# Kernel tuning notes

Hardware: AMD Instinct MI355X
Metric: run time of the kernel (lower is better)

## Reference

```python
import jax, jax.numpy as jnp
import numpy as np

D_MODEL = 512
NHEAD = 8
HEAD_DIM = D_MODEL // NHEAD


def setup_inputs() -> dict:
    key = jax.random.key(0)
    k1, k2, k3, k4, k5 = jax.random.split(key, 5)
    x = jax.random.normal(k1, (4, 2048, D_MODEL), dtype=jnp.float32)
    s = 1.0 / np.sqrt(D_MODEL)
    W_qkv = jax.random.normal(k2, (D_MODEL, 3 * D_MODEL), dtype=jnp.float32) * s
    b_qkv = jax.random.normal(k3, (3 * D_MODEL,), dtype=jnp.float32) * 0.01
    W_fc = jax.random.normal(k4, (D_MODEL, D_MODEL), dtype=jnp.float32) * s
    b_fc = jax.random.normal(k5, (D_MODEL,), dtype=jnp.float32) * 0.01
    return {"x": x, "W_qkv": W_qkv, "b_qkv": b_qkv, "W_fc": W_fc, "b_fc": b_fc}


def reference(x, W_qkv, b_qkv, W_fc, b_fc):
    b, t, _ = x.shape
    qkv = x @ W_qkv + b_qkv                      # [b, t, 3*d]
    q, k, v = jnp.split(qkv, 3, axis=-1)
    def heads(a):
        return a.reshape(b, t, NHEAD, HEAD_DIM).transpose(0, 2, 1, 3)  # b h t d
    q, k, v = heads(q), heads(k), heads(v)
    scale = HEAD_DIM ** -0.5
    dots = jnp.einsum('bhid,bhjd->bhij', q, k) * scale
    attn = jax.nn.softmax(dots, axis=-1)         # dropout = identity (eval)
    out = jnp.einsum('bhij,bhjd->bhid', attn, v)
    out = out.transpose(0, 2, 1, 3).reshape(b, t, D_MODEL)
    return out @ W_fc + b_fc
```

## Files before the change

### kernel.cpp

```cpp
#include <hip/hip_runtime.h>
#include <hip/hip_bf16.h>
#include <cstddef>
#include <cstdint>

typedef __bf16 bf16_t;
typedef __attribute__((ext_vector_type(8))) __bf16 bf16x8;
typedef __attribute__((ext_vector_type(4))) float f32x4;
typedef __attribute__((ext_vector_type(16))) float f32x16;
typedef __attribute__((ext_vector_type(2))) unsigned uint2v;

#define B_   4
#define T_   2048
#define D_   512
#define H_   8
#define HD_  64
#define BT_  8192
#define N3_  1536

__device__ inline f32x4 mfma16(bf16x8 a, bf16x8 b, f32x4 c) {
  return __builtin_amdgcn_mfma_f32_16x16x32_bf16(a, b, c, 0, 0, 0);
}
__device__ inline f32x16 mfma32(bf16x8 a, bf16x8 b, f32x16 c) {
  return __builtin_amdgcn_mfma_f32_32x32x16_bf16(a, b, c, 0, 0, 0);
}


__global__ __launch_bounds__(256) void k_tcast(const float* __restrict__ in,
                                               bf16_t* __restrict__ out,
                                               int R, int C) {
  __shared__ bf16_t tile[64][72];
  const int c0 = blockIdx.x * 64, r0 = blockIdx.y * 64;
  const int t = threadIdx.x;
  const int rr = t >> 4;
  const int cc = (t & 15) * 4;
#pragma unroll
  for (int p = 0; p < 4; ++p) {
    int r = p * 16 + rr;
    f32x4 v = *reinterpret_cast<const f32x4*>(&in[(size_t)(r0 + r) * C + c0 + cc]);
#pragma unroll
    for (int i = 0; i < 4; ++i) tile[cc + i][r] = (bf16_t)v[i];
  }
  __syncthreads();
#pragma unroll
  for (int p = 0; p < 4; ++p) {
    int c = p * 16 + rr;
    union { uint2 u; bf16_t e[4]; } pk;
#pragma unroll
    for (int i = 0; i < 4; ++i) pk.e[i] = tile[c][cc + i];
    *reinterpret_cast<uint2*>(&out[(size_t)(c0 + c) * R + r0 + cc]) = pk.u;
  }
}

__global__ __launch_bounds__(256) void k_gemm_qkv(
    const float* __restrict__ X, const bf16_t* __restrict__ Wt,
    const float* __restrict__ bias, bf16_t* __restrict__ Qp,
    bf16_t* __restrict__ Kp, bf16_t* __restrict__ Vp) {
  __shared__ bf16_t As[128][40];
  __shared__ bf16_t Bs[128][40];
  const int bm0 = blockIdx.x * 128, bn0 = blockIdx.y * 128;
  const int tid = threadIdx.x, lane = tid & 63, wid = tid >> 6;
  const int wm = wid >> 1, wn = wid & 1;
  const int srow = tid >> 1, sh = (tid & 1) * 16;
  f32x4 acc[4][4] = {};
  for (int kt = 0; kt < D_; kt += 32) {
    {
      const float* s = &X[(size_t)(bm0 + srow) * D_ + kt + sh];
      f32x4 v0 = *reinterpret_cast<const f32x4*>(s);
      f32x4 v1 = *reinterpret_cast<const f32x4*>(s + 4);
      f32x4 v2 = *reinterpret_cast<const f32x4*>(s + 8);
      f32x4 v3 = *reinterpret_cast<const f32x4*>(s + 12);
      bf16x8 lo, hi;
#pragma unroll
      for (int i = 0; i < 4; ++i) {
        lo[i] = (bf16_t)v0[i]; lo[4 + i] = (bf16_t)v1[i];
        hi[i] = (bf16_t)v2[i]; hi[4 + i] = (bf16_t)v3[i];
      }
      *reinterpret_cast<bf16x8*>(&As[srow][sh]) = lo;
      *reinterpret_cast<bf16x8*>(&As[srow][sh + 8]) = hi;
    }
    {
      const bf16_t* s = &Wt[(size_t)(bn0 + srow) * D_ + kt + sh];
      *reinterpret_cast<bf16x8*>(&Bs[srow][sh]) =
          *reinterpret_cast<const bf16x8*>(s);
      *reinterpret_cast<bf16x8*>(&Bs[srow][sh + 8]) =
          *reinterpret_cast<const bf16x8*>(s + 8);
    }
    __syncthreads();
    const int fr = lane & 15, kq = (lane >> 4) * 8;
    bf16x8 af[4], bfr[4];
#pragma unroll
    for (int m = 0; m < 4; ++m)
      af[m] = *reinterpret_cast<const bf16x8*>(&As[wm * 64 + m * 16 + fr][kq]);
#pragma unroll
    for (int n = 0; n < 4; ++n)
      bfr[n] = *reinterpret_cast<const bf16x8*>(&Bs[wn * 64 + n * 16 + fr][kq]);
#pragma unroll
    for (int m = 0; m < 4; ++m)
#pragma unroll
      for (int n = 0; n < 4; ++n)
        acc[m][n] = mfma16(af[m], bfr[n], acc[m][n]);
    __syncthreads();
  }
  const float c1 = 0.18033688011112042f;
  const int fr = lane & 15, fq = lane >> 4;
#pragma unroll
  for (int n = 0; n < 4; ++n) {
    int ng = bn0 + wn * 64 + n * 16 + fr;
    float bv = bias[ng];
    int sec = ng >> 9, ns = ng & 511;
    int h = ns >> 6, d = ns & 63;
#pragma unroll
    for (int m = 0; m < 4; ++m) {
      int mg = bm0 + wm * 64 + m * 16 + fq * 4;
#pragma unroll
      for (int j = 0; j < 4; ++j) {
        int row = mg + j;
        int bb = row >> 11, tt = row & 2047;
        int bh = bb * H_ + h;
        float fv = acc[m][n][j] + bv;
        if (sec == 2) {
          size_t a = (((size_t)(bh * 128 + (tt >> 4)) * 2 + (d >> 5)) << 9) +
                     (size_t)((d & 31) + 32 * ((tt >> 3) & 1)) * 8 + (tt & 7);
          Vp[a] = (bf16_t)fv;
        } else {
          size_t a = (((size_t)(bh * 64 + (tt >> 5)) * 4 + (d >> 4)) << 9) +
                     (size_t)((tt & 31) + 32 * ((d >> 3) & 1)) * 8 + (d & 7);
          (sec == 0 ? Qp : Kp)[a] = (bf16_t)(sec == 0 ? fv * c1 : fv);
        }
      }
    }
  }
}

__global__ __launch_bounds__(256) void k_gemm_fc(
    const bf16_t* __restrict__ A, const bf16_t* __restrict__ Wt,
    const float* __restrict__ bias, float* __restrict__ Out) {
  __shared__ bf16_t As[128][40];
  __shared__ bf16_t Bs[128][40];
  const int bm0 = blockIdx.x * 128, bn0 = blockIdx.y * 128;
  const int tid = threadIdx.x, lane = tid & 63, wid = tid >> 6;
  const int wm = wid >> 1, wn = wid & 1;
  const int srow = tid >> 1, sh = (tid & 1) * 16;
  f32x4 acc[4][4] = {};
  for (int kt = 0; kt < D_; kt += 32) {
    {
      const bf16_t* s = &A[(size_t)(bm0 + srow) * D_ + kt + sh];
      *reinterpret_cast<bf16x8*>(&As[srow][sh]) =
          *reinterpret_cast<const bf16x8*>(s);
      *reinterpret_cast<bf16x8*>(&As[srow][sh + 8]) =
          *reinterpret_cast<const bf16x8*>(s + 8);
    }
    {
      const bf16_t* s = &Wt[(size_t)(bn0 + srow) * D_ + kt + sh];
      *reinterpret_cast<bf16x8*>(&Bs[srow][sh]) =
          *reinterpret_cast<const bf16x8*>(s);
      *reinterpret_cast<bf16x8*>(&Bs[srow][sh + 8]) =
          *reinterpret_cast<const bf16x8*>(s + 8);
    }
    __syncthreads();
    const int fr = lane & 15, kq = (lane >> 4) * 8;
    bf16x8 af[4], bfr[4];
#pragma unroll
    for (int m = 0; m < 4; ++m)
      af[m] = *reinterpret_cast<const bf16x8*>(&As[wm * 64 + m * 16 + fr][kq]);
#pragma unroll
    for (int n = 0; n < 4; ++n)
      bfr[n] = *reinterpret_cast<const bf16x8*>(&Bs[wn * 64 + n * 16 + fr][kq]);
#pragma unroll
    for (int m = 0; m < 4; ++m)
#pragma unroll
      for (int n = 0; n < 4; ++n)
        acc[m][n] = mfma16(af[m], bfr[n], acc[m][n]);
    __syncthreads();
  }
  const int fr = lane & 15, fq = lane >> 4;
#pragma unroll
  for (int n = 0; n < 4; ++n) {
    int ng = bn0 + wn * 64 + n * 16 + fr;
    float bv = bias[ng];
#pragma unroll
    for (int m = 0; m < 4; ++m) {
      int mg = bm0 + wm * 64 + m * 16 + fq * 4;
#pragma unroll
      for (int j = 0; j < 4; ++j)
        Out[(size_t)(mg + j) * D_ + ng] = acc[m][n][j] + bv;
    }
  }
}

__device__ __forceinline__ void loadKf(const bf16_t* __restrict__ b, int tile,
                                       bf16x8 (&kf)[4]) {
#pragma unroll
  for (int ds = 0; ds < 4; ++ds)
    kf[ds] = *reinterpret_cast<const bf16x8*>(b + ((size_t)(tile * 4 + ds) << 9));
}
__device__ __forceinline__ void loadVf(const bf16_t* __restrict__ b, int c0,
                                       bf16x8 (&v)[4]) {
  v[0] = *reinterpret_cast<const bf16x8*>(b + ((size_t)(c0 * 2 + 0) << 9));
  v[1] = *reinterpret_cast<const bf16x8*>(b + ((size_t)(c0 * 2 + 2) << 9));
  v[2] = *reinterpret_cast<const bf16x8*>(b + ((size_t)(c0 * 2 + 1) << 9));
  v[3] = *reinterpret_cast<const bf16x8*>(b + ((size_t)(c0 * 2 + 3) << 9));
}

__device__ __forceinline__ f32x16 qk32(const bf16x8 (&kf)[4],
                                       const bf16x8 (&qf)[4]) {
  f32x16 s;
#pragma unroll
  for (int i = 0; i < 16; ++i) s[i] = 0.f;
  s = mfma32(kf[0], qf[0], s);
  s = mfma32(kf[1], qf[1], s);
  s = mfma32(kf[2], qf[2], s);
  s = mfma32(kf[3], qf[3], s);
  return s;
}

__device__ __forceinline__ void pv_acc(f32x16& s, const bf16x8 (&v)[4],
                                       f32x16& o0, f32x16& o1, float& lsum) {
  float p[16];
#pragma unroll
  for (int r = 0; r < 16; ++r) p[r] = __builtin_exp2f(s[r]);
  lsum += (((p[0] + p[1]) + (p[2] + p[3])) + ((p[4] + p[5]) + (p[6] + p[7]))) +
          (((p[8] + p[9]) + (p[10] + p[11])) +
           ((p[12] + p[13]) + (p[14] + p[15])));
  union PW { __hip_bfloat162 h; unsigned u; };
#pragma unroll
  for (int ks = 0; ks < 2; ++ks) {
    const int rb = ks * 8;
    PW t0, t1, t2, t3;
    t0.h = __float22bfloat162_rn(make_float2(p[rb + 0], p[rb + 1]));
    t1.h = __float22bfloat162_rn(make_float2(p[rb + 2], p[rb + 3]));
    t2.h = __float22bfloat162_rn(make_float2(p[rb + 4], p[rb + 5]));
    t3.h = __float22bfloat162_rn(make_float2(p[rb + 6], p[rb + 7]));
    uint2v r02 = __builtin_amdgcn_permlane32_swap(t0.u, t2.u, false, false);
    uint2v r13 = __builtin_amdgcn_permlane32_swap(t1.u, t3.u, false, false);
    union { unsigned u[4]; bf16x8 vv; } af;
    af.u[0] = r02[0]; af.u[1] = r13[0]; af.u[2] = r02[1]; af.u[3] = r13[1];
    if (ks == 0) {
      o0 = mfma32(af.vv, v[0], o0);
      o1 = mfma32(af.vv, v[2], o1);
    } else {
      o0 = mfma32(af.vv, v[1], o0);
      o1 = mfma32(af.vv, v[3], o1);
    }
  }
}

__global__ __launch_bounds__(512, 2) void k_attn(
    const bf16_t* __restrict__ Qp, const bf16_t* __restrict__ Kp,
    const bf16_t* __restrict__ Vp, bf16_t* __restrict__ Ctx) {
  __shared__ float Olds[4][32][64];
  __shared__ float Llds[4][64];
  const int lin = blockIdx.x;
  const int logical = (lin & 7) * 64 + (lin >> 3);
  const int bh = logical >> 4, qblk = logical & 15;
  const int tid = threadIdx.x, lane = tid & 63, wid = tid >> 6;
  const int qt = wid & 3, half = wid >> 2;
  const int q0 = qblk * 128 + qt * 32;
  const int tbase = half * 32;
  const bf16_t* Qb = Qp + ((size_t)(bh * 64 + (q0 >> 5)) << 11) + lane * 8;
  const bf16_t* Kb = Kp + ((size_t)bh << 17) + lane * 8;
  const bf16_t* Vb = Vp + ((size_t)bh << 17) + lane * 8;
  bf16x8 qf[4];
#pragma unroll
  for (int ds = 0; ds < 4; ++ds)
    qf[ds] = *reinterpret_cast<const bf16x8*>(Qb + ((size_t)ds << 9));
  f32x16 o0, o1;
#pragma unroll
  for (int i = 0; i < 16; ++i) { o0[i] = 0.f; o1[i] = 0.f; }
  float lsum = 0.f;
  bf16x8 kfA[4], kfB[4], vA[4], vB[4];
  loadKf(Kb, tbase + 0, kfA);
  loadKf(Kb, tbase + 1, kfB);
  loadVf(Vb, (tbase << 1) + 0, vA);
  loadVf(Vb, (tbase << 1) + 2, vB);
  f32x16 sA = qk32(kfA, qf);
  for (int st = 0; st < 32; st += 2) {
    const bool more = (st + 2 < 32);
    f32x16 sB = qk32(kfB, qf);
    if (more) loadKf(Kb, tbase + st + 2, kfA);
    pv_acc(sA, vA, o0, o1, lsum);
    if (more) loadVf(Vb, ((tbase + st) << 1) + 4, vA);
    if (more) sA = qk32(kfA, qf);
    if (more) loadKf(Kb, tbase + st + 3, kfB);
    pv_acc(sB, vB, o0, o1, lsum);
    if (more) loadVf(Vb, ((tbase + st) << 1) + 6, vB);
  }
  lsum += __shfl_xor(lsum, 32);
  if (half == 1) {
#pragma unroll
    for (int r = 0; r < 16; ++r) {
      Olds[qt][r][lane] = o0[r];
      Olds[qt][16 + r][lane] = o1[r];
    }
    Llds[qt][lane] = lsum;
  }
  __syncthreads();
  if (half == 1) return;
  const float lfull = lsum + Llds[qt][lane];
  const float linv = 1.f / lfull;
  const int bb = bh >> 3, hh = bh & 7;
  const int ql = lane & 31;
#pragma unroll
  for (int r = 0; r < 16; ++r) {
    const int qr = (r & 3) + 8 * (r >> 2) + 4 * (lane >> 5);
    const float li = __shfl(linv, qr);
    float v0 = (o0[r] + Olds[qt][r][lane]) * li;
    float v1 = (o1[r] + Olds[qt][16 + r][lane]) * li;
    size_t base = ((size_t)(bb * T_ + q0 + qr)) * D_ + hh * HD_ + ql;
    Ctx[base] = (bf16_t)v0;
    Ctx[base + 32] = (bf16_t)v1;
  }
}

extern "C" void kernel_launch(void* const* d_in, const int* in_sizes, int n_in,
                              void* d_out, int out_size, void* d_ws,
                              size_t ws_size, hipStream_t stream) {
  const float* x    = (const float*)d_in[0];
  const float* Wqkv = (const float*)d_in[1];
  const float* bqkv = (const float*)d_in[2];
  const float* Wfc  = (const float*)d_in[3];
  const float* bfc  = (const float*)d_in[4];
  float* out = (float*)d_out;

  char* ws = (char*)d_ws;
  size_t off = 0;
  bf16_t* Wqt = (bf16_t*)(ws + off); off += (size_t)N3_ * D_ * 2;
  bf16_t* Wft = (bf16_t*)(ws + off); off += (size_t)D_ * D_ * 2;
  bf16_t* Qb  = (bf16_t*)(ws + off); off += (size_t)BT_ * D_ * 2;
  bf16_t* Kb  = (bf16_t*)(ws + off); off += (size_t)BT_ * D_ * 2;
  bf16_t* Vb  = (bf16_t*)(ws + off); off += (size_t)BT_ * D_ * 2;
  bf16_t* Ctx = (bf16_t*)(ws + off); off += (size_t)BT_ * D_ * 2;

  k_tcast<<<dim3(N3_ / 64, D_ / 64), 256, 0, stream>>>(Wqkv, Wqt, D_, N3_);
  k_tcast<<<dim3(D_ / 64, D_ / 64), 256, 0, stream>>>(Wfc, Wft, D_, D_);
  k_gemm_qkv<<<dim3(BT_ / 128, N3_ / 128), 256, 0, stream>>>(x, Wqt, bqkv, Qb,
                                                             Kb, Vb);
  k_attn<<<512, 512, 0, stream>>>(Qb, Kb, Vb, Ctx);
  k_gemm_fc<<<dim3(BT_ / 128, D_ / 128), 256, 0, stream>>>(Ctx, Wft, bfc, out);
}
```

Baseline: 113.1 us.

## Pre-cast X to bf16 and stage GEMM tiles via direct global-to-LDS loads

Adds a separate kernel that casts X from fp32 to bf16 once, placing it in the Ctx buffer, so the QKV GEMM reads bf16 instead of converting fp32 per tile. Both GEMMs now fill LDS with global_load_lds instead of going through registers, and drop the padded LDS rows for a dense 32-wide layout. The aim is less VGPR traffic and less load instruction overhead. In exchange there is an extra launch, an extra write and read of X, and likely LDS bank conflicts on the fragment reads now that the padding is gone.

```diff
diff --git a/kernel.cpp b/kernel.cpp
--- a/kernel.cpp
+++ b/kernel.cpp
@@ -24,6 +24,22 @@
   return __builtin_amdgcn_mfma_f32_32x32x16_bf16(a, b, c, 0, 0, 0);
 }
 
+#define GLOADLDS(lds_base, gsrc)                                           \
+  __builtin_amdgcn_global_load_lds(                                        \
+      (const __attribute__((address_space(1))) unsigned int*)(gsrc),       \
+      (__attribute__((address_space(3))) unsigned int*)(lds_base), 16, 0, 0)
+
+
+__global__ __launch_bounds__(256) void k_castx(const float* __restrict__ in,
+                                               bf16_t* __restrict__ out) {
+  const size_t i = ((size_t)blockIdx.x * 256 + threadIdx.x) * 8;
+  f32x4 v0 = *reinterpret_cast<const f32x4*>(&in[i]);
+  f32x4 v1 = *reinterpret_cast<const f32x4*>(&in[i + 4]);
+  bf16x8 o;
+#pragma unroll
+  for (int k = 0; k < 4; ++k) { o[k] = (bf16_t)v0[k]; o[4 + k] = (bf16_t)v1[k]; }
+  *reinterpret_cast<bf16x8*>(&out[i]) = o;
+}
 
 __global__ __launch_bounds__(256) void k_tcast(const float* __restrict__ in,
                                                bf16_t* __restrict__ out,
@@ -52,48 +68,35 @@
 }
 
 __global__ __launch_bounds__(256) void k_gemm_qkv(
-    const float* __restrict__ X, const bf16_t* __restrict__ Wt,
+    const bf16_t* __restrict__ Xb, const bf16_t* __restrict__ Wt,
     const float* __restrict__ bias, bf16_t* __restrict__ Qp,
     bf16_t* __restrict__ Kp, bf16_t* __restrict__ Vp) {
-  __shared__ bf16_t As[128][40];
-  __shared__ bf16_t Bs[128][40];
+  __shared__ __align__(16) bf16_t As[128 * 32];
+  __shared__ __align__(16) bf16_t Bs[128 * 32];
   const int bm0 = blockIdx.x * 128, bn0 = blockIdx.y * 128;
   const int tid = threadIdx.x, lane = tid & 63, wid = tid >> 6;
   const int wm = wid >> 1, wn = wid & 1;
-  const int srow = tid >> 1, sh = (tid & 1) * 16;
+  const int srow = lane >> 2;
+  const int scol = (lane & 3) * 8;
   f32x4 acc[4][4] = {};
   for (int kt = 0; kt < D_; kt += 32) {
-    {
-      const float* s = &X[(size_t)(bm0 + srow) * D_ + kt + sh];
-      f32x4 v0 = *reinterpret_cast<const f32x4*>(s);
-      f32x4 v1 = *reinterpret_cast<const f32x4*>(s + 4);
-      f32x4 v2 = *reinterpret_cast<const f32x4*>(s + 8);
-      f32x4 v3 = *reinterpret_cast<const f32x4*>(s + 12);
-      bf16x8 lo, hi;
-#pragma unroll
-      for (int i = 0; i < 4; ++i) {
-        lo[i] = (bf16_t)v0[i]; lo[4 + i] = (bf16_t)v1[i];
-        hi[i] = (bf16_t)v2[i]; hi[4 + i] = (bf16_t)v3[i];
-      }
-      *reinterpret_cast<bf16x8*>(&As[srow][sh]) = lo;
-      *reinterpret_cast<bf16x8*>(&As[srow][sh + 8]) = hi;
-    }
-    {
-      const bf16_t* s = &Wt[(size_t)(bn0 + srow) * D_ + kt + sh];
-      *reinterpret_cast<bf16x8*>(&Bs[srow][sh]) =
-          *reinterpret_cast<const bf16x8*>(s);
-      *reinterpret_cast<bf16x8*>(&Bs[srow][sh + 8]) =
-          *reinterpret_cast<const bf16x8*>(s + 8);
+#pragma unroll
+    for (int i = 0; i < 2; ++i) {
+      const int r = 32 * wid + 16 * i + srow;
+      GLOADLDS(&As[(32 * wid + 16 * i) * 32],
+               &Xb[(size_t)(bm0 + r) * D_ + kt + scol]);
+      GLOADLDS(&Bs[(32 * wid + 16 * i) * 32],
+               &Wt[(size_t)(bn0 + r) * D_ + kt + scol]);
     }
     __syncthreads();
     const int fr = lane & 15, kq = (lane >> 4) * 8;
     bf16x8 af[4], bfr[4];
 #pragma unroll
     for (int m = 0; m < 4; ++m)
-      af[m] = *reinterpret_cast<const bf16x8*>(&As[wm * 64 + m * 16 + fr][kq]);
+      af[m] = *reinterpret_cast<const bf16x8*>(&As[(wm * 64 + m * 16 + fr) * 32 + kq]);
 #pragma unroll
     for (int n = 0; n < 4; ++n)
-      bfr[n] = *reinterpret_cast<const bf16x8*>(&Bs[wn * 64 + n * 16 + fr][kq]);
+      bfr[n] = *reinterpret_cast<const bf16x8*>(&Bs[(wn * 64 + n * 16 + fr) * 32 + kq]);
 #pragma unroll
     for (int m = 0; m < 4; ++m)
 #pragma unroll
@@ -135,37 +138,32 @@
 __global__ __launch_bounds__(256) void k_gemm_fc(
     const bf16_t* __restrict__ A, const bf16_t* __restrict__ Wt,
     const float* __restrict__ bias, float* __restrict__ Out) {
-  __shared__ bf16_t As[128][40];
-  __shared__ bf16_t Bs[128][40];
+  __shared__ __align__(16) bf16_t As[128 * 32];
+  __shared__ __align__(16) bf16_t Bs[128 * 32];
   const int bm0 = blockIdx.x * 128, bn0 = blockIdx.y * 128;
   const int tid = threadIdx.x, lane = tid & 63, wid = tid >> 6;
   const int wm = wid >> 1, wn = wid & 1;
-  const int srow = tid >> 1, sh = (tid & 1) * 16;
+  const int srow = lane >> 2;
+  const int scol = (lane & 3) * 8;
   f32x4 acc[4][4] = {};
   for (int kt = 0; kt < D_; kt += 32) {
-    {
-      const bf16_t* s = &A[(size_t)(bm0 + srow) * D_ + kt + sh];
-      *reinterpret_cast<bf16x8*>(&As[srow][sh]) =
-          *reinterpret_cast<const bf16x8*>(s);
-      *reinterpret_cast<bf16x8*>(&As[srow][sh + 8]) =
-          *reinterpret_cast<const bf16x8*>(s + 8);
-    }
-    {
-      const bf16_t* s = &Wt[(size_t)(bn0 + srow) * D_ + kt + sh];
-      *reinterpret_cast<bf16x8*>(&Bs[srow][sh]) =
-          *reinterpret_cast<const bf16x8*>(s);
-      *reinterpret_cast<bf16x8*>(&Bs[srow][sh + 8]) =
-          *reinterpret_cast<const bf16x8*>(s + 8);
+#pragma unroll
+    for (int i = 0; i < 2; ++i) {
+      const int r = 32 * wid + 16 * i + srow;
+      GLOADLDS(&As[(32 * wid + 16 * i) * 32],
+               &A[(size_t)(bm0 + r) * D_ + kt + scol]);
+      GLOADLDS(&Bs[(32 * wid + 16 * i) * 32],
+               &Wt[(size_t)(bn0 + r) * D_ + kt + scol]);
     }
     __syncthreads();
     const int fr = lane & 15, kq = (lane >> 4) * 8;
     bf16x8 af[4], bfr[4];
 #pragma unroll
     for (int m = 0; m < 4; ++m)
-      af[m] = *reinterpret_cast<const bf16x8*>(&As[wm * 64 + m * 16 + fr][kq]);
+      af[m] = *reinterpret_cast<const bf16x8*>(&As[(wm * 64 + m * 16 + fr) * 32 + kq]);
 #pragma unroll
     for (int n = 0; n < 4; ++n)
-      bfr[n] = *reinterpret_cast<const bf16x8*>(&Bs[wn * 64 + n * 16 + fr][kq]);
+      bfr[n] = *reinterpret_cast<const bf16x8*>(&Bs[(wn * 64 + n * 16 + fr) * 32 + kq]);
 #pragma unroll
     for (int m = 0; m < 4; ++m)
 #pragma unroll
@@ -330,10 +328,12 @@
   bf16_t* Kb  = (bf16_t*)(ws + off); off += (size_t)BT_ * D_ * 2;
   bf16_t* Vb  = (bf16_t*)(ws + off); off += (size_t)BT_ * D_ * 2;
   bf16_t* Ctx = (bf16_t*)(ws + off); off += (size_t)BT_ * D_ * 2;
-
+  bf16_t* Xb  = Ctx;
+
+  k_castx<<<BT_ * D_ / (256 * 8), 256, 0, stream>>>(x, Xb);
   k_tcast<<<dim3(N3_ / 64, D_ / 64), 256, 0, stream>>>(Wqkv, Wqt, D_, N3_);
   k_tcast<<<dim3(D_ / 64, D_ / 64), 256, 0, stream>>>(Wfc, Wft, D_, D_);
-  k_gemm_qkv<<<dim3(BT_ / 128, N3_ / 128), 256, 0, stream>>>(x, Wqt, bqkv, Qb,
+  k_gemm_qkv<<<dim3(BT_ / 128, N3_ / 128), 256, 0, stream>>>(Xb, Wqt, bqkv, Qb,
                                                              Kb, Vb);
   k_attn<<<512, 512, 0, stream>>>(Qb, Kb, Vb, Ctx);
   k_gemm_fc<<<dim3(BT_ / 128, D_ / 128), 256, 0, stream>>>(Ctx, Wft, bfc, out);
```

Measured after the change: 109.1 us. 1.04x faster.
